# Kernel optimization log

Measured on AMD Instinct MI355X. Metric: run time of the kernel, lower is better.

The kernel has to match this reference:

```python
import jax, jax.numpy as jnp
import numpy as np

B, L, H, D = 2, 1024, 8, 64
DIM = H * D


def setup_inputs() -> dict:
    key = jax.random.key(0)
    ks = jax.random.split(key, 12)
    s = 0.02  # weight init scale
    return {
        "x": jax.random.normal(ks[0], (B, L, DIM), dtype=jnp.float32),
        "wq_w": jax.random.normal(ks[1], (DIM, DIM), dtype=jnp.float32) * s,
        "wq_b": jax.random.normal(ks[2], (DIM,), dtype=jnp.float32) * s,
        "wk_w": jax.random.normal(ks[3], (DIM, DIM), dtype=jnp.float32) * s,
        "wk_b": jax.random.normal(ks[4], (DIM,), dtype=jnp.float32) * s,
        "wv_w": jax.random.normal(ks[5], (DIM, DIM), dtype=jnp.float32) * s,
        "wv_b": jax.random.normal(ks[6], (DIM,), dtype=jnp.float32) * s,
        "phazor_re": jax.random.normal(ks[7], (H, D), dtype=jnp.float32),
        "phazor_im": jax.random.normal(ks[8], (H, D), dtype=jnp.float32),
        "amplitude": jax.random.normal(ks[9], (H,), dtype=jnp.float32),
        "last_conv_re": jax.random.normal(ks[10], (H, D, D), dtype=jnp.float32),
        "last_conv_im": jax.random.normal(ks[11], (H, D, D), dtype=jnp.float32),
    }


def reference(x, wq_w, wq_b, wk_w, wk_b, wv_w, wv_b,
              phazor_re, phazor_im, amplitude, last_conv_re, last_conv_im):
    b, l, _ = x.shape
    h, d = phazor_re.shape
    cplx = jnp.complex64

    q = (x @ wq_w.T + wq_b).reshape(b, l, h, d)
    k = (x @ wk_w.T + wk_b).reshape(b, l, h, d)
    v = (x @ wv_w.T + wv_b).reshape(b, l, h, d)

    phazor_p = (phazor_re + 1j * phazor_im).astype(cplx)      # (H,D)
    phase = phazor_p / jnp.abs(phazor_p)                      # unit-modulus
    amp = jax.nn.sigmoid(amplitude)                           # (H,)
    phazor = phase * amp[:, None]                             # (H,D)

    t = jnp.arange(l)
    phase_prog = phase[None] ** t[:, None, None]              # (L,H,D)
    phase_prog_inv = phase[None] ** (-t)[:, None, None]       # (L,H,D)
    phazor_prog = phazor[None] ** t[:, None, None]            # (L,H,D)

    # cross-chunk: q_t * phazor^{t+1} contracted with initial state (detached)
    last_conv = (last_conv_re + 1j * last_conv_im).astype(cplx)  # (H,D,D)
    qc = q.astype(cplx) * (phazor_prog * phazor[None])[None]     # (B,L,H,D)
    cross = jnp.einsum('blhd,hde->blhe', qc, last_conv)          # (B,L,H,D)

    # decay mask: amp^(i-j) on the lower triangle
    diff = t[:, None] - t[None, :]
    tril = diff >= 0
    mask = jnp.where(tril[None],
                     amp[:, None, None] ** jnp.where(tril, diff, 0)[None],
                     0.0)                                        # (H,L,L)

    qph = q.astype(cplx) * phase_prog[None]                      # (B,L,H,D)
    kph = k.astype(cplx) * phase_prog_inv[None]                  # (B,L,H,D)
    qk = jnp.einsum('blhd,bmhd->bhlm', qph, kph)                 # (B,H,L,L) complex
    qk_mask = qk * mask[None].astype(cplx)
    inner = jnp.einsum('bhlm,bmhd->blhd', qk_mask, v.astype(cplx))

    out = (inner + cross).real.astype(x.dtype).reshape(b, l, h * d)
    return out
```

## Files before the change

### kernel.cpp

```cpp
#include <hip/hip_runtime.h>
#include <hip/hip_bf16.h>
#include <math.h>

#define L_SEQ 1024
#define DIMSZ 512
#define NH 8
#define ND 64
#define NB 2
#define CHUNK 64
#define NC (L_SEQ / CHUNK)
#define BHTOT (NB * NH)
#define MTOT 2048
#define KEFF 512
#define BM 64
#define BN 128

#define SWZ(row, col) ((col) ^ (((row) & 7) << 3))

typedef __attribute__((ext_vector_type(8))) _Float16 f16x8;
typedef __attribute__((ext_vector_type(4))) float f32x4;

#define GLD16(g, l) __builtin_amdgcn_global_load_lds( \
    (const __attribute__((address_space(1))) unsigned int*)(g), \
    (__attribute__((address_space(3))) unsigned int*)(l), 16, 0, 0)

__device__ static inline unsigned short f2h(float f) {
    union { _Float16 h; unsigned short u; } x;
    x.h = (_Float16)f;
    return x.u;
}
__device__ static inline float h2f(unsigned short u) {
    union { unsigned short u; _Float16 h; } x;
    x.u = u;
    return (float)x.h;
}
__device__ static inline unsigned packh2(float a, float b) {
    return (unsigned)f2h(a) | ((unsigned)f2h(b) << 16);
}

__global__ __launch_bounds__(256) void pack_kernel(
    const float* __restrict__ x,
    const float* __restrict__ wq, const float* __restrict__ wk, const float* __restrict__ wv,
    const float* __restrict__ lc_re, const float* __restrict__ lc_im,
    unsigned short* __restrict__ A, unsigned short* __restrict__ Bm,
    unsigned* __restrict__ lcT)
{
    __shared__ unsigned T[64][65];
    const int bid = blockIdx.x;
    const int tid = threadIdx.x;
    if (bid < 1024) {
        const int i = bid * 256 + tid;
        const int n  = i >> 7;
        const int kq = (i & 127) << 2;
        const float4 xv = *(const float4*)(x + (size_t)n * DIMSZ + kq);
        *(ushort4*)(A + (size_t)n * KEFF + kq) =
            make_ushort4(f2h(xv.x), f2h(xv.y), f2h(xv.z), f2h(xv.w));
    } else if (bid < 1792) {
        const int idx = bid - 1024;
        const int which = idx >> 8;
        const float* w = which == 0 ? wq : (which == 1 ? wk : wv);
        const int i = (idx & 255) * 256 + tid;
        const int o  = i >> 7;
        const int kq = (i & 127) << 2;
        const float4 wv4 = *(const float4*)(w + (size_t)o * DIMSZ + kq);
        const int row = (which == 0) ? o
                      : 512 + (which - 1) * 64 + (o >> 6) * 128 + (o & 63);
        *(ushort4*)(Bm + (size_t)row * KEFF + kq) =
            make_ushort4(f2h(wv4.x), f2h(wv4.y), f2h(wv4.z), f2h(wv4.w));
    } else {
        const int h = bid - 1792;
        const int e = tid & 63;
        #pragma unroll
        for (int i = 0; i < 16; ++i) {
            const int d = i*4 + (tid >> 6);
            T[e][d] = packh2(lc_re[h*4096 + d*64 + e], lc_im[h*4096 + d*64 + e]);
        }
        __syncthreads();
        const int d = tid & 63;
        #pragma unroll
        for (int i = 0; i < 16; ++i) {
            const int e2 = i*4 + (tid >> 6);
            lcT[h*4096 + e2*64 + d] = T[e2][d];
        }
    }
}

__global__ __launch_bounds__(256) void gemm_kv_kernel(
    const unsigned short* __restrict__ A, const unsigned short* __restrict__ Bm,
    const float* __restrict__ bq, const float* __restrict__ bk, const float* __restrict__ bv,
    const float* __restrict__ ph_re, const float* __restrict__ ph_im,
    const float* __restrict__ ampl,
    unsigned short* __restrict__ qo, unsigned short* __restrict__ ko,
    unsigned short* __restrict__ vo, unsigned* __restrict__ kvB)
{
    __shared__ __align__(16) char lds[49152];
    const int tid  = threadIdx.x;
    const int lane = tid & 63;
    const int wave = tid >> 6;

    const int bid0 = blockIdx.x;
    int sw;
    if (bid0 < 256) sw = 128 + ((bid0 & 7) * 32 + (bid0 >> 3));
    else            { const int r = bid0 - 256; sw = (r & 7) * 16 + (r >> 3); }
    const bool isQ = sw < 128;
    int mtile, brow0, h = 0, panel = 0;
    if (isQ) { panel = sw & 3; mtile = sw >> 2; brow0 = panel * 128; }
    else     { const int r = sw - 128; h = r & 7; mtile = r >> 3; brow0 = 512 + h * 128; }
    const int row0 = mtile * 64;
    const int wr = wave >> 1, wc = wave & 1;

    const int srow = tid >> 3;
    const int sin  = (tid & 7) << 4;
    size_t goffA[2], goffB[4];
    #pragma unroll
    for (int c = 0; c < 2; ++c) {
        const int row = c * 32 + srow;
        const int swz = sin ^ ((row & 7) << 4);
        goffA[c] = (size_t)(row0 + row) * (KEFF * 2) + swz;
    }
    #pragma unroll
    for (int c = 0; c < 4; ++c) {
        const int row = c * 32 + srow;
        const int swz = sin ^ ((row & 7) << 4);
        goffB[c] = (size_t)(brow0 + row) * (KEFF * 2) + swz;
    }
    const int ldst = tid * 16;
    const char* Abyte = (const char*)A;
    const char* Bbyte = (const char*)Bm;

    f32x4 acc[2][4];
    const f32x4 zf = {0.f, 0.f, 0.f, 0.f};
    #pragma unroll
    for (int m = 0; m < 2; ++m)
        #pragma unroll
        for (int n = 0; n < 4; ++n) acc[m][n] = zf;

    auto stage = [&](int buf, int t) {
        char* la = lds + buf * 24576;
        char* lb = la + 8192;
        const size_t kb = (size_t)t * 128;
        #pragma unroll
        for (int c = 0; c < 2; ++c)
            GLD16(Abyte + goffA[c] + kb, la + c * 4096 + ldst);
        #pragma unroll
        for (int c = 0; c < 4; ++c)
            GLD16(Bbyte + goffB[c] + kb, lb + c * 4096 + ldst);
    };

    const int rl = lane & 15;
    const int kg = lane >> 4;
    const int rswz = (rl & 7) << 4;

    auto compute = [&](int buf) {
        const char* la = lds + buf * 24576;
        const char* lb = la + 8192;
        #pragma unroll
        for (int ks = 0; ks < 2; ++ks) {
            f16x8 av[2], bvv[4];
            #pragma unroll
            for (int m = 0; m < 2; ++m) {
                const int row = wr * 32 + m * 16 + rl;
                const int addr = (row * 128 + ks * 64 + kg * 16) ^ rswz;
                av[m] = *(const f16x8*)(la + addr);
            }
            #pragma unroll
            for (int n = 0; n < 4; ++n) {
                const int row = wc * 64 + n * 16 + rl;
                const int addr = (row * 128 + ks * 64 + kg * 16) ^ rswz;
                bvv[n] = *(const f16x8*)(lb + addr);
            }
            #pragma unroll
            for (int m = 0; m < 2; ++m)
                #pragma unroll
                for (int n = 0; n < 4; ++n)
                    acc[m][n] = __builtin_amdgcn_mfma_f32_16x16x32_f16(
                        av[m], bvv[n], acc[m][n], 0, 0, 0);
        }
    };

    stage(0, 0);
    __syncthreads();
    const int NT = KEFF / 64;
    for (int t = 0; t < NT; ++t) {
        if (t + 1 < NT) stage((t + 1) & 1, t + 1);
        compute(t & 1);
        __syncthreads();
    }

    if (isQ) {
        #pragma unroll
        for (int n = 0; n < 4; ++n) {
            const int cabs = panel * 128 + wc * 64 + n * 16 + rl;
            const float bs = bq[cabs];
            #pragma unroll
            for (int m = 0; m < 2; ++m) {
                const int rb = row0 + wr * 32 + m * 16 + kg * 4;
                #pragma unroll
                for (int r = 0; r < 4; ++r)
                    qo[(size_t)(rb + r) * DIMSZ + cabs] = f2h(acc[m][n][r] + bs);
            }
        }
        return;
    }

    _Float16 (*KTR)[64] = (_Float16(*)[64])(lds);
    _Float16 (*KTI)[64] = (_Float16(*)[64])(lds + 8192);
    _Float16 (*VWT)[64] = (_Float16(*)[64])(lds + 16384);

    unsigned short* outp = wc == 0 ? ko : vo;
    _Float16 (*RAW)[64] = wc == 0 ? KTR : VWT;
    #pragma unroll
    for (int n = 0; n < 4; ++n) {
        const int cl = h * 64 + n * 16 + rl;
        const int drow = n * 16 + rl;
        const float bs = (wc == 0 ? bk : bv)[cl];
        #pragma unroll
        for (int m = 0; m < 2; ++m) {
            const int jb = wr * 32 + m * 16 + kg * 4;
            #pragma unroll
            for (int r = 0; r < 4; ++r) {
                const float val = acc[m][n][r] + bs;
                outp[(size_t)(row0 + jb + r) * DIMSZ + cl] = f2h(val);
                RAW[drow][SWZ(drow, jb + r)] = (_Float16)val;
            }
        }
    }
    __syncthreads();

    const float amp = 1.0f / (1.0f + expf(-ampl[h]));
    const float la_ = logf(amp);
    const float th = atan2f(ph_im[h*ND + lane], ph_re[h*ND + lane]);
    float sth2, cth2; sincosf(th, &sth2, &cth2);
    const float p0 = (float)(CHUNK - 1 - (wave*16 + 15));
    float ap = expf(la_ * p0);
    float sp, cp; sincosf(th * p0, &sp, &cp);
    #pragma unroll
    for (int jj = 15; jj >= 0; --jj) {
        const int j = wave*16 + jj;
        const int cj = SWZ(lane, j);
        const float kk = (float)KTR[lane][cj];
        const float vv = (float)VWT[lane][cj];
        KTR[lane][cj] = (_Float16)(kk * cp);
        KTI[lane][cj] = (_Float16)(kk * sp);
        VWT[lane][cj] = (_Float16)(vv * ap);
        const float ncp = cp*cth2 - sp*sth2;
        sp = cp*sth2 + sp*cth2; cp = ncp;
        ap *= amp;
    }
    __syncthreads();

    const int b = mtile >> 4, c = mtile & 15;
    unsigned* dst = kvB + (size_t)(((b * NH + h) << 4) | c) * (ND * ND);
    #pragma unroll
    for (int i = 0; i < 4; ++i) {
        const int mt = wave, nt = i;
        f32x4 aR = zf, aI = zf;
        const int mrow = mt*16 + rl, nrow = nt*16 + rl;
        #pragma unroll
        for (int ks = 0; ks < 2; ++ks) {
            const f16x8 av = *(const f16x8*)&VWT[mrow][SWZ(mrow, ks*32 + kg*8)];
            const f16x8 br = *(const f16x8*)&KTR[nrow][SWZ(nrow, ks*32 + kg*8)];
            const f16x8 bi = *(const f16x8*)&KTI[nrow][SWZ(nrow, ks*32 + kg*8)];
            aR = __builtin_amdgcn_mfma_f32_16x16x32_f16(av, br, aR, 0, 0, 0);
            aI = __builtin_amdgcn_mfma_f32_16x16x32_f16(av, bi, aI, 0, 0, 0);
        }
        const int d = nt*16 + rl;
        #pragma unroll
        for (int r = 0; r < 4; ++r) {
            const int e = mt*16 + kg*4 + r;
            dst[e*ND + d] = packh2(aR[r], aI[r]);
        }
    }
}

__global__ __launch_bounds__(256) void scan_kernel(
    unsigned* __restrict__ kvB, const unsigned* __restrict__ lcT,
    const float* __restrict__ ph_re, const float* __restrict__ ph_im,
    const float* __restrict__ ampl)
{
    const int gid = blockIdx.x * 256 + threadIdx.x;
    const int bh = gid >> 12;
    const int idx = gid & 4095;
    const int h = bh & 7;
    const int d = idx & 63;

    const float th = atan2f(ph_im[h*ND + d], ph_re[h*ND + d]);
    const float la = -logf(1.0f + expf(-ampl[h]));
    const float ampC = expf(la * (float)CHUNK);
    float s, ct; sincosf(th * (float)CHUNK, &s, &ct);
    const float aCr = ampC * ct, aCi = ampC * s;

    unsigned* base = kvB + (size_t)bh * NC * (ND*ND) + idx;
    unsigned tl[NC];
    #pragma unroll
    for (int cc = 0; cc < NC; ++cc) tl[cc] = base[(size_t)cc * (ND*ND)];

    const unsigned lcp = lcT[h*4096 + idx];
    float Sr = h2f((unsigned short)(lcp & 0xffffu));
    float Si = h2f((unsigned short)(lcp >> 16));
    #pragma unroll
    for (int cc = 0; cc < NC; ++cc) {
        base[(size_t)cc * (ND*ND)] = packh2(Sr, Si);
        const float tr = h2f((unsigned short)(tl[cc] & 0xffffu));
        const float ti = h2f((unsigned short)(tl[cc] >> 16));
        const float nr = aCr*Sr - aCi*Si + tr;
        const float ni = aCr*Si + aCi*Sr + ti;
        Sr = nr; Si = ni;
    }
}

__global__ __launch_bounds__(512) void chunk_out_kernel(
    const unsigned short* __restrict__ q, const unsigned short* __restrict__ k,
    const unsigned short* __restrict__ v, const unsigned* __restrict__ Bst,
    const float* __restrict__ ph_re, const float* __restrict__ ph_im,
    const float* __restrict__ ampl, float* __restrict__ out)
{
    __shared__ __align__(16) _Float16 QhR[64][64], QhI[64][64];
    __shared__ __align__(16) _Float16 KhR[64][64], KhI[64][64];
    __shared__ __align__(16) _Float16 VT[64][64];
    __shared__ __align__(16) _Float16 SA[64][64];
    __shared__ float apw[80];

    const int bhc = blockIdx.x;
    const int c  = bhc & (NC - 1);
    const int bh = bhc >> 4;
    const int b = bh >> 3, h = bh & 7;
    const int tid = threadIdx.x;
    const int lane = tid & 63, w = tid >> 6;
    const int rl = lane & 15, kg = lane >> 4;
    const int rt = w >> 1;

    const float la = -logf(1.0f + expf(-ampl[h]));
    if (tid < 72) apw[tid] = expf(la * (float)tid);
    const float th = atan2f(ph_im[h*ND + lane], ph_re[h*ND + lane]);
    float sth_, cth_; sincosf(th, &sth_, &cth_);

    unsigned breg[8];
    const unsigned* Bb = Bst + (size_t)bhc * (ND*ND);
    #pragma unroll
    for (int ii = 0; ii < 8; ++ii) breg[ii] = Bb[ii*512 + tid];

    {
        const int jbase = w * 8;
        float sr, cr; sincosf(th * (float)jbase, &sr, &cr);
        #pragma unroll
        for (int jj = 0; jj < 8; ++jj) {
            const int j = jbase + jj;
            const size_t off = ((size_t)(b*L_SEQ + c*CHUNK + j)) * DIMSZ + h*ND + lane;
            const float qq = h2f(q[off]);
            const float kk = h2f(k[off]);
            const int cl = SWZ(j, lane);
            QhR[j][cl] = (_Float16)(qq * cr);
            QhI[j][cl] = (_Float16)(qq * sr);
            KhR[j][cl] = (_Float16)(kk * cr);
            KhI[j][cl] = (_Float16)(kk * sr);
            VT[lane][SWZ(lane, j)] = (_Float16)h2f(v[off]);
            const float ncr = cr*cth_ - sr*sth_;
            sr = cr*sth_ + sr*cth_; cr = ncr;
        }
    }
    __syncthreads();

    const f32x4 zf = {0.f, 0.f, 0.f, 0.f};
    f32x4 sacc[2] = {zf, zf};
    #pragma unroll
    for (int t = 0; t < 2; ++t) {
        const int nt = (w & 1)*2 + t;
        if (rt >= nt) {
            const int arow = rt*16 + rl, brow = nt*16 + rl;
            #pragma unroll
            for (int ks = 0; ks < 2; ++ks) {
                const f16x8 aR = *(const f16x8*)&QhR[arow][SWZ(arow, ks*32 + kg*8)];
                const f16x8 bR = *(const f16x8*)&KhR[brow][SWZ(brow, ks*32 + kg*8)];
                sacc[t] = __builtin_amdgcn_mfma_f32_16x16x32_f16(aR, bR, sacc[t], 0, 0, 0);
                const f16x8 aI = *(const f16x8*)&QhI[arow][SWZ(arow, ks*32 + kg*8)];
                const f16x8 bI = *(const f16x8*)&KhI[brow][SWZ(brow, ks*32 + kg*8)];
                sacc[t] = __builtin_amdgcn_mfma_f32_16x16x32_f16(aI, bI, sacc[t], 0, 0, 0);
            }
        }
    }
    __syncthreads();

    #pragma unroll
    for (int t = 0; t < 2; ++t) {
        const int nt = (w & 1)*2 + t;
        #pragma unroll
        for (int r = 0; r < 4; ++r) {
            const int rowm = rt*16 + kg*4 + r;
            const int jp = nt*16 + rl;
            const int delta = rowm - jp;
            const float val = (delta >= 0) ? sacc[t][r] * apw[delta] : 0.0f;
            SA[rowm][SWZ(rowm, jp)] = (_Float16)val;
        }
    }
    #pragma unroll
    for (int ii = 0; ii < 8; ++ii) {
        const int e = ii*8 + w;
        const float br = h2f((unsigned short)(breg[ii] & 0xffffu));
        const float bi = h2f((unsigned short)(breg[ii] >> 16));
        const int cl = SWZ(e, lane);
        KhR[e][cl] = (_Float16)(br*cth_ - bi*sth_);
        KhI[e][cl] = (_Float16)(-(br*sth_ + bi*cth_));
    }
    __syncthreads();

    #pragma unroll
    for (int t = 0; t < 2; ++t) {
        const int nt = (w & 1)*2 + t;
        f32x4 accO = zf, accC = zf;
        const int arow = rt*16 + rl, brow = nt*16 + rl;
        #pragma unroll
        for (int ks = 0; ks < 2; ++ks) {
            const f16x8 aS = *(const f16x8*)&SA[arow][SWZ(arow, ks*32 + kg*8)];
            const f16x8 bV = *(const f16x8*)&VT[brow][SWZ(brow, ks*32 + kg*8)];
            accO = __builtin_amdgcn_mfma_f32_16x16x32_f16(aS, bV, accO, 0, 0, 0);
            const f16x8 aR = *(const f16x8*)&QhR[arow][SWZ(arow, ks*32 + kg*8)];
            const f16x8 bBR = *(const f16x8*)&KhR[brow][SWZ(brow, ks*32 + kg*8)];
            accC = __builtin_amdgcn_mfma_f32_16x16x32_f16(aR, bBR, accC, 0, 0, 0);
            const f16x8 aI = *(const f16x8*)&QhI[arow][SWZ(arow, ks*32 + kg*8)];
            const f16x8 bBI = *(const f16x8*)&KhI[brow][SWZ(brow, ks*32 + kg*8)];
            accC = __builtin_amdgcn_mfma_f32_16x16x32_f16(aI, bBI, accC, 0, 0, 0);
        }
        const int e = nt*16 + rl;
        #pragma unroll
        for (int r = 0; r < 4; ++r) {
            const int rowm = rt*16 + kg*4 + r;
            const float cs = apw[rowm + 1];
            out[((size_t)(b*L_SEQ + c*CHUNK + rowm)) * DIMSZ + h*ND + e] =
                accO[r] + cs * accC[r];
        }
    }
}

extern "C" void kernel_launch(void* const* d_in, const int* in_sizes, int n_in,
                              void* d_out, int out_size, void* d_ws, size_t ws_size,
                              hipStream_t stream)
{
    const float* x     = (const float*)d_in[0];
    const float* wq_w  = (const float*)d_in[1];
    const float* wq_b  = (const float*)d_in[2];
    const float* wk_w  = (const float*)d_in[3];
    const float* wk_b  = (const float*)d_in[4];
    const float* wv_w  = (const float*)d_in[5];
    const float* wv_b  = (const float*)d_in[6];
    const float* ph_re = (const float*)d_in[7];
    const float* ph_im = (const float*)d_in[8];
    const float* ampl  = (const float*)d_in[9];
    const float* lc_re = (const float*)d_in[10];
    const float* lc_im = (const float*)d_in[11];
    float* out = (float*)d_out;

    char* wsb = (char*)d_ws;
    const size_t MB = 1024 * 1024;
    unsigned short* q = (unsigned short*)(wsb + 0);
    unsigned short* k = (unsigned short*)(wsb + 2 * MB);
    unsigned short* v = (unsigned short*)(wsb + 4 * MB);
    unsigned* kvB = (unsigned*)(wsb + 8 * MB);
    unsigned short* Apk = (unsigned short*)(wsb + 13 * MB);
    unsigned short* Bpk = (unsigned short*)(wsb + 16 * MB);
    unsigned* lcT = (unsigned*)(wsb + 18 * MB);

    pack_kernel<<<1800, 256, 0, stream>>>(
        x, wq_w, wk_w, wv_w, lc_re, lc_im, Apk, Bpk, lcT);
    gemm_kv_kernel<<<384, 256, 0, stream>>>(
        Apk, Bpk, wq_b, wk_b, wv_b, ph_re, ph_im, ampl, q, k, v, kvB);
    scan_kernel<<<256, 256, 0, stream>>>(kvB, lcT, ph_re, ph_im, ampl);
    chunk_out_kernel<<<BHTOT * NC, 512, 0, stream>>>(
        q, k, v, kvB, ph_re, ph_im, ampl, out);
}
```

Baseline: 32.45 us.

## Fuse Q projection into per-head KV GEMM tiles with 192-wide N

Reorders the packed weight matrix so each head owns a contiguous 192-row panel (Q, K, V interleaved), and widens the GEMM N tile from 128 to 192 so one block computes Q, K and V for a head and row tile. This removes the separate Q-only blocks, cutting the grid from 384 to 256 blocks and reusing each loaded A tile across all three projections. In exchange it uses 64KB of LDS per block and more accumulator registers, which may lower occupancy, and the epilogue now branches per column group.

```diff
diff --git a/kernel.cpp b/kernel.cpp
--- a/kernel.cpp
+++ b/kernel.cpp
@@ -12,8 +12,6 @@
 #define BHTOT (NB * NH)
 #define MTOT 2048
 #define KEFF 512
-#define BM 64
-#define BN 128
 
 #define SWZ(row, col) ((col) ^ (((row) & 7) << 3))
 
@@ -63,8 +61,7 @@
         const int o  = i >> 7;
         const int kq = (i & 127) << 2;
         const float4 wv4 = *(const float4*)(w + (size_t)o * DIMSZ + kq);
-        const int row = (which == 0) ? o
-                      : 512 + (which - 1) * 64 + (o >> 6) * 128 + (o & 63);
+        const int row = (o >> 6) * 192 + which * 64 + (o & 63);
         *(ushort4*)(Bm + (size_t)row * KEFF + kq) =
             make_ushort4(f2h(wv4.x), f2h(wv4.y), f2h(wv4.z), f2h(wv4.w));
     } else {
@@ -93,25 +90,21 @@
     unsigned short* __restrict__ qo, unsigned short* __restrict__ ko,
     unsigned short* __restrict__ vo, unsigned* __restrict__ kvB)
 {
-    __shared__ __align__(16) char lds[49152];
+    __shared__ __align__(16) char lds[65536];
     const int tid  = threadIdx.x;
     const int lane = tid & 63;
     const int wave = tid >> 6;
 
     const int bid0 = blockIdx.x;
-    int sw;
-    if (bid0 < 256) sw = 128 + ((bid0 & 7) * 32 + (bid0 >> 3));
-    else            { const int r = bid0 - 256; sw = (r & 7) * 16 + (r >> 3); }
-    const bool isQ = sw < 128;
-    int mtile, brow0, h = 0, panel = 0;
-    if (isQ) { panel = sw & 3; mtile = sw >> 2; brow0 = panel * 128; }
-    else     { const int r = sw - 128; h = r & 7; mtile = r >> 3; brow0 = 512 + h * 128; }
+    const int sw = (bid0 & 7) * 32 + (bid0 >> 3);
+    const int mtile = sw >> 3, h = sw & 7;
     const int row0 = mtile * 64;
+    const int brow0 = h * 192;
     const int wr = wave >> 1, wc = wave & 1;
 
     const int srow = tid >> 3;
     const int sin  = (tid & 7) << 4;
-    size_t goffA[2], goffB[4];
+    size_t goffA[2], goffB[6];
     #pragma unroll
     for (int c = 0; c < 2; ++c) {
         const int row = c * 32 + srow;
@@ -119,7 +112,7 @@
         goffA[c] = (size_t)(row0 + row) * (KEFF * 2) + swz;
     }
     #pragma unroll
-    for (int c = 0; c < 4; ++c) {
+    for (int c = 0; c < 6; ++c) {
         const int row = c * 32 + srow;
         const int swz = sin ^ ((row & 7) << 4);
         goffB[c] = (size_t)(brow0 + row) * (KEFF * 2) + swz;
@@ -128,22 +121,22 @@
     const char* Abyte = (const char*)A;
     const char* Bbyte = (const char*)Bm;
 
-    f32x4 acc[2][4];
+    f32x4 acc[2][6];
     const f32x4 zf = {0.f, 0.f, 0.f, 0.f};
     #pragma unroll
     for (int m = 0; m < 2; ++m)
         #pragma unroll
-        for (int n = 0; n < 4; ++n) acc[m][n] = zf;
+        for (int n = 0; n < 6; ++n) acc[m][n] = zf;
 
     auto stage = [&](int buf, int t) {
-        char* la = lds + buf * 24576;
+        char* la = lds + buf * 32768;
         char* lb = la + 8192;
         const size_t kb = (size_t)t * 128;
         #pragma unroll
         for (int c = 0; c < 2; ++c)
             GLD16(Abyte + goffA[c] + kb, la + c * 4096 + ldst);
         #pragma unroll
-        for (int c = 0; c < 4; ++c)
+        for (int c = 0; c < 6; ++c)
             GLD16(Bbyte + goffB[c] + kb, lb + c * 4096 + ldst);
     };
 
@@ -152,11 +145,11 @@
     const int rswz = (rl & 7) << 4;
 
     auto compute = [&](int buf) {
-        const char* la = lds + buf * 24576;
+        const char* la = lds + buf * 32768;
         const char* lb = la + 8192;
         #pragma unroll
         for (int ks = 0; ks < 2; ++ks) {
-            f16x8 av[2], bvv[4];
+            f16x8 av[2], bvv[6];
             #pragma unroll
             for (int m = 0; m < 2; ++m) {
                 const int row = wr * 32 + m * 16 + rl;
@@ -164,15 +157,15 @@
                 av[m] = *(const f16x8*)(la + addr);
             }
             #pragma unroll
-            for (int n = 0; n < 4; ++n) {
-                const int row = wc * 64 + n * 16 + rl;
+            for (int n = 0; n < 6; ++n) {
+                const int row = wc * 96 + n * 16 + rl;
                 const int addr = (row * 128 + ks * 64 + kg * 16) ^ rswz;
                 bvv[n] = *(const f16x8*)(lb + addr);
             }
             #pragma unroll
             for (int m = 0; m < 2; ++m)
                 #pragma unroll
-                for (int n = 0; n < 4; ++n)
+                for (int n = 0; n < 6; ++n)
                     acc[m][n] = __builtin_amdgcn_mfma_f32_16x16x32_f16(
                         av[m], bvv[n], acc[m][n], 0, 0, 0);
         }
@@ -187,33 +180,21 @@
         __syncthreads();
     }
 
-    if (isQ) {
-        #pragma unroll
-        for (int n = 0; n < 4; ++n) {
-            const int cabs = panel * 128 + wc * 64 + n * 16 + rl;
-            const float bs = bq[cabs];
-            #pragma unroll
-            for (int m = 0; m < 2; ++m) {
-                const int rb = row0 + wr * 32 + m * 16 + kg * 4;
-                #pragma unroll
-                for (int r = 0; r < 4; ++r)
-                    qo[(size_t)(rb + r) * DIMSZ + cabs] = f2h(acc[m][n][r] + bs);
-            }
-        }
-        return;
-    }
-
     _Float16 (*KTR)[64] = (_Float16(*)[64])(lds);
     _Float16 (*KTI)[64] = (_Float16(*)[64])(lds + 8192);
     _Float16 (*VWT)[64] = (_Float16(*)[64])(lds + 16384);
 
-    unsigned short* outp = wc == 0 ? ko : vo;
-    _Float16 (*RAW)[64] = wc == 0 ? KTR : VWT;
-    #pragma unroll
-    for (int n = 0; n < 4; ++n) {
-        const int cl = h * 64 + n * 16 + rl;
-        const int drow = n * 16 + rl;
-        const float bs = (wc == 0 ? bk : bv)[cl];
+    #pragma unroll
+    for (int n = 0; n < 6; ++n) {
+        const int colp = wc * 96 + n * 16;
+        const int which = colp >> 6;
+        const int d0 = colp & 63;
+        const float* bias = which == 0 ? bq : (which == 1 ? bk : bv);
+        unsigned short* outp = which == 0 ? qo : (which == 1 ? ko : vo);
+        const int d = d0 + rl;
+        const int cl = h * 64 + d;
+        const float bs = bias[cl];
+        _Float16 (*RAW)[64] = which == 1 ? KTR : VWT;
         #pragma unroll
         for (int m = 0; m < 2; ++m) {
             const int jb = wr * 32 + m * 16 + kg * 4;
@@ -221,7 +202,8 @@
             for (int r = 0; r < 4; ++r) {
                 const float val = acc[m][n][r] + bs;
                 outp[(size_t)(row0 + jb + r) * DIMSZ + cl] = f2h(val);
-                RAW[drow][SWZ(drow, jb + r)] = (_Float16)val;
+                if (which != 0)
+                    RAW[d][SWZ(d, jb + r)] = (_Float16)val;
             }
         }
     }
@@ -462,7 +444,7 @@
 
     pack_kernel<<<1800, 256, 0, stream>>>(
         x, wq_w, wk_w, wv_w, lc_re, lc_im, Apk, Bpk, lcT);
-    gemm_kv_kernel<<<384, 256, 0, stream>>>(
+    gemm_kv_kernel<<<256, 256, 0, stream>>>(
         Apk, Bpk, wq_b, wk_b, wv_b, ph_re, ph_im, ampl, q, k, v, kvB);
     scan_kernel<<<256, 256, 0, stream>>>(kvB, lcT, ph_re, ph_im, ampl);
     chunk_out_kernel<<<BHTOT * NC, 512, 0, stream>>>(
```

Result: slower. 34.70 us (+6.9%).
